# Optimization experiments

Hardware: AMD Instinct MI355X
Metric: run time of the kernel (lower is better)

The kernel has to match this reference:

```python
import jax, jax.numpy as jnp
import numpy as np

E = 8
D_IN = 1024
D_HID = 4096
D_OUT = 1024
N_TOK = 32768  # total tokens; equal split of 4096 per expert


def setup_inputs() -> dict:
    key = jax.random.key(0)
    k_in, k_w1, k_w2 = jax.random.split(key, 3)
    inputs = jax.random.normal(k_in, (N_TOK, D_IN), dtype=jnp.float32)
    expert_size = jnp.full((E,), N_TOK // E, dtype=jnp.int64)
    # reset_parameters: normal(0, 1/sqrt(fan_in)) per expert
    w1 = jax.random.normal(k_w1, (E, D_IN, D_HID), dtype=jnp.float32) / np.sqrt(D_IN)
    b1 = jnp.zeros((E, D_HID), dtype=jnp.float32)
    w2 = jax.random.normal(k_w2, (E, D_HID, D_OUT), dtype=jnp.float32) / np.sqrt(D_HID)
    b2 = jnp.zeros((E, D_OUT), dtype=jnp.float32)
    return {"inputs": inputs, "expert_size": expert_size,
            "w1": w1, "b1": b1, "w2": w2, "b2": b2}


def reference(inputs, expert_size, w1, b1, w2, b2):
    # Grouped GEMM over contiguous per-expert splits. expert_size is equal
    # per expert (N_TOK // E), so the variable-split loop in the torch code
    # collapses to a batched einsum with identical math.
    e = w1.shape[0]
    n, d = inputs.shape
    cap = n // e  # tokens per expert (equal splits)
    x = inputs.reshape(e, cap, d)                       # [E, cap, D_IN]
    h = jnp.einsum('ecd,edh->ech', x, w1) + b1[:, None, :]
    h = jax.nn.gelu(h, approximate=False)               # F.gelu default = erf gelu
    y = jnp.einsum('ech,eho->eco', h, w2) + b2[:, None, :]
    return y.reshape(n, -1)                             # [N_TOK, D_OUT]
```

## Files before the change

kernel.cpp:

```cpp
#include <hip/hip_runtime.h>
#include <hip/hip_bf16.h>
#include <type_traits>

#define NE 8
#define DIN 1024
#define DHID 4096
#define DOUTD 1024
#define NTOK 32768
#define CAP (NTOK / NE)

typedef unsigned short u16;
typedef __attribute__((ext_vector_type(8))) short bf16x8;
typedef __attribute__((ext_vector_type(4))) float f32x4;

template <int I> using ic = std::integral_constant<int, I>;

__device__ __forceinline__ u16 f2bf(float x) {
  unsigned u = __builtin_bit_cast(unsigned, x);
  u += 0x7fffu + ((u >> 16) & 1u);
  return (u16)(u >> 16);
}

__device__ __forceinline__ float gelu_f(float x) {
  float u = 0.7978845608028654f * x * (1.0f + 0.044715f * x * x);
  float t = __expf(-2.0f * fabsf(u));
  float r = __fdividef(2.0f * t, 1.0f + t);
  float th = copysignf(1.0f - r, u);
  return 0.5f * x * (1.0f + th);
}

__device__ __forceinline__ void async_ld16(const void* g, void* l) {
  __builtin_amdgcn_global_load_lds(
      (const __attribute__((address_space(1))) unsigned int*)g,
      (__attribute__((address_space(3))) unsigned int*)l, 16, 0, 0);
}

__global__ __launch_bounds__(256) void convert_bf16_kernel(const float* __restrict__ in,
                                                           u16* __restrict__ out) {
  size_t i = ((size_t)blockIdx.x * 256 + threadIdx.x) * 8;
  float4 a = *(const float4*)(in + i);
  float4 b = *(const float4*)(in + i + 4);
  uint4 o;
  o.x = (unsigned)f2bf(a.x) | ((unsigned)f2bf(a.y) << 16);
  o.y = (unsigned)f2bf(a.z) | ((unsigned)f2bf(a.w) << 16);
  o.z = (unsigned)f2bf(b.x) | ((unsigned)f2bf(b.y) << 16);
  o.w = (unsigned)f2bf(b.z) | ((unsigned)f2bf(b.w) << 16);
  *(uint4*)(out + i) = o;
}

__global__ __launch_bounds__(256) void transpose_bf16_kernel(const float* __restrict__ in,
                                                             u16* __restrict__ out,
                                                             int K, int N) {
  __shared__ __align__(16) u16 tile[64 * 72];
  const int e = blockIdx.z;
  const int n0 = blockIdx.x * 64;
  const int k0 = blockIdx.y * 64;
  const float* inp = in + (size_t)e * K * N;
  u16* outp = out + (size_t)e * N * K;
  const int t = threadIdx.x;
  const int kr = t >> 4;
  const int nc = (t & 15) * 4;
#pragma unroll
  for (int rr = 0; rr < 4; ++rr) {
    int kl = rr * 16 + kr;
    float4 v = *(const float4*)(inp + (size_t)(k0 + kl) * N + n0 + nc);
    tile[(nc + 0) * 72 + kl] = f2bf(v.x);
    tile[(nc + 1) * 72 + kl] = f2bf(v.y);
    tile[(nc + 2) * 72 + kl] = f2bf(v.z);
    tile[(nc + 3) * 72 + kl] = f2bf(v.w);
  }
  __syncthreads();
  const int nr = t >> 3;
  const int kc = (t & 7) * 8;
#pragma unroll
  for (int it = 0; it < 2; ++it) {
    int nl = it * 32 + nr;
    bf16x8 w = *(const bf16x8*)(tile + nl * 72 + kc);
    *(bf16x8*)(outp + (size_t)(n0 + nl) * K + k0 + kc) = w;
  }
}

template <int K, int N, bool GELU_OUT>
__global__ __launch_bounds__(256, 2) void moe_gemm128_kernel(
    const u16* __restrict__ A, const u16* __restrict__ Bt,
    const float* __restrict__ bias, void* __restrict__ Out) {
  extern __shared__ __align__(16) char smem_raw[];
  constexpr int TX = N / 128;
  constexpr int NT = K / 64;
  static_assert(NT % 2 == 0 && NT >= 4, "K-tile count");
  static_assert(TX % 8 == 0, "supertile map needs TX%8==0");

  const int bid = blockIdx.x;
  const int e = bid & 7;
  const int idx = bid >> 3;
  constexpr int STC = TX / 8;
  const int st = idx >> 6;
  const int win = idx & 63;
  const int m0 = ((st / STC) * 8 + (win >> 3)) * 128;
  const int n0 = ((st % STC) * 8 + (win & 7)) * 128;

  const u16* Ae = A + (size_t)e * CAP * K;
  const u16* Be = Bt + (size_t)e * N * K;

  const int tid = threadIdx.x;
  const int l = tid & 63;
  const int w = tid >> 6;
  const int wr = w >> 1;
  const int wc = w & 1;
  const int g = l >> 4;
  const int rl = l & 15;

  int aoff0[4], aoff1[4], boff0[4], boff1[4];
#pragma unroll
  for (int j = 0; j < 4; ++j) {
    int r = wr * 64 + j * 16 + rl;
    aoff0[j] = r * 128 + (((0 * 4 + g) ^ (r & 7)) << 4);
    aoff1[j] = r * 128 + (((1 * 4 + g) ^ (r & 7)) << 4);
  }
#pragma unroll
  for (int i = 0; i < 4; ++i) {
    int r = wc * 64 + i * 16 + rl;
    boff0[i] = 16384 + r * 128 + (((0 * 4 + g) ^ (r & 7)) << 4);
    boff1[i] = 16384 + r * 128 + (((1 * 4 + g) ^ (r & 7)) << 4);
  }

  auto mkoff = [&](int s, int base0) -> size_t {
    int lrow = s >> 3, pu = s & 7;
    int lu = pu ^ (lrow & 7);
    return (size_t)(base0 + lrow) * K + lu * 8;
  };
  const u16* pA[4];
  const u16* pB[4];
#pragma unroll
  for (int r = 0; r < 4; ++r) {
    pA[r] = Ae + mkoff(r * 256 + tid, m0);
    pB[r] = Be + mkoff(r * 256 + tid, n0);
  }
  const int dsl = tid * 16;

  f32x4 acc[4][4] = {};

#pragma unroll
  for (int r = 0; r < 4; ++r) async_ld16(pA[r], smem_raw + r * 4096 + dsl);
#pragma unroll
  for (int r = 0; r < 4; ++r) async_ld16(pB[r], smem_raw + 16384 + r * 4096 + dsl);
  asm volatile("s_waitcnt vmcnt(0)\n\ts_barrier" ::: "memory");
  __builtin_amdgcn_sched_barrier(0);

  auto tile = [&](auto Jc, auto STc, auto LASTc) {
    constexpr int J = decltype(Jc)::value;
    constexpr bool STg = decltype(STc)::value;
    constexpr bool LAST = decltype(LASTc)::value;
    const char* bufr = smem_raw + J * 32768;
    char* bufs = (char*)smem_raw + (J ^ 1) * 32768;
    const int stE = (J + 1) * 64;
    if constexpr (STg) {
#pragma unroll
      for (int r = 0; r < 4; ++r) async_ld16(pA[r] + stE, bufs + r * 4096 + dsl);
#pragma unroll
      for (int r = 0; r < 4; ++r) async_ld16(pB[r] + stE, bufs + 16384 + r * 4096 + dsl);
    }
    bf16x8 b0[4], a0[4], b1[4], a1[4];
#pragma unroll
    for (int i = 0; i < 4; ++i) b0[i] = *(const bf16x8*)(bufr + boff0[i]);
#pragma unroll
    for (int j = 0; j < 4; ++j) a0[j] = *(const bf16x8*)(bufr + aoff0[j]);
#pragma unroll
    for (int i = 0; i < 4; ++i) b1[i] = *(const bf16x8*)(bufr + boff1[i]);
#pragma unroll
    for (int j = 0; j < 4; ++j) a1[j] = *(const bf16x8*)(bufr + aoff1[j]);
    asm volatile("s_waitcnt lgkmcnt(8)" ::: "memory");
    __builtin_amdgcn_sched_barrier(0);
    __builtin_amdgcn_s_setprio(1);
#pragma unroll
    for (int j = 0; j < 4; ++j)
#pragma unroll
      for (int i = 0; i < 4; ++i)
        acc[j][i] = __builtin_amdgcn_mfma_f32_16x16x32_bf16(b0[i], a0[j], acc[j][i], 0, 0, 0);
    asm volatile("s_waitcnt lgkmcnt(0)" ::: "memory");
    __builtin_amdgcn_sched_barrier(0);
#pragma unroll
    for (int j = 0; j < 4; ++j)
#pragma unroll
      for (int i = 0; i < 4; ++i)
        acc[j][i] = __builtin_amdgcn_mfma_f32_16x16x32_bf16(b1[i], a1[j], acc[j][i], 0, 0, 0);
    __builtin_amdgcn_s_setprio(0);
    if constexpr (!LAST) {
      asm volatile("s_waitcnt vmcnt(0)\n\ts_barrier" ::: "memory");
      __builtin_amdgcn_sched_barrier(0);
    }
  };

#pragma unroll 1
  for (int pr = 0; pr < NT / 2 - 1; ++pr) {
    tile(ic<0>{}, std::true_type{}, std::false_type{});
    tile(ic<1>{}, std::true_type{}, std::false_type{});
#pragma unroll
    for (int r = 0; r < 4; ++r) { pA[r] += 128; pB[r] += 128; }
  }
  tile(ic<0>{}, std::true_type{}, std::false_type{});
  tile(ic<1>{}, std::false_type{}, std::true_type{});

  const float* be = bias + (size_t)e * N;
  const int mb = m0 + wr * 64 + rl;
  const int nb = n0 + wc * 64 + g * 4;
  if constexpr (GELU_OUT) {
    u16* Oe = (u16*)Out + (size_t)e * (size_t)CAP * N;
#pragma unroll
    for (int j = 0; j < 4; ++j) {
      int m = mb + j * 16;
#pragma unroll
      for (int i = 0; i < 4; ++i) {
        int n = nb + i * 16;
        float4 bv = *(const float4*)(be + n);
        ushort4 o;
        o.x = f2bf(gelu_f(acc[j][i][0] + bv.x));
        o.y = f2bf(gelu_f(acc[j][i][1] + bv.y));
        o.z = f2bf(gelu_f(acc[j][i][2] + bv.z));
        o.w = f2bf(gelu_f(acc[j][i][3] + bv.w));
        *(ushort4*)(Oe + (size_t)m * N + n) = o;
      }
    }
  } else {
    float* Oe = (float*)Out + (size_t)e * (size_t)CAP * N;
#pragma unroll
    for (int j = 0; j < 4; ++j) {
      int m = mb + j * 16;
#pragma unroll
      for (int i = 0; i < 4; ++i) {
        int n = nb + i * 16;
        float4 bv = *(const float4*)(be + n);
        float4 o;
        o.x = acc[j][i][0] + bv.x;
        o.y = acc[j][i][1] + bv.y;
        o.z = acc[j][i][2] + bv.z;
        o.w = acc[j][i][3] + bv.w;
        *(float4*)(Oe + (size_t)m * N + n) = o;
      }
    }
  }
}

extern "C" void kernel_launch(void* const* d_in, const int* in_sizes, int n_in,
                              void* d_out, int out_size, void* d_ws, size_t ws_size,
                              hipStream_t stream) {
  const float* x  = (const float*)d_in[0];
  const float* w1 = (const float*)d_in[2];
  const float* b1 = (const float*)d_in[3];
  const float* w2 = (const float*)d_in[4];
  const float* b2 = (const float*)d_in[5];
  float* out = (float*)d_out;

  char* wsp = (char*)d_ws;
  u16* x_bf = (u16*)(wsp);
  u16* w1t  = (u16*)(wsp + (size_t)67108864);
  u16* w2t  = (u16*)(wsp + (size_t)134217728);
  u16* h    = (u16*)(wsp + (size_t)201326592);

  hipFuncSetAttribute(reinterpret_cast<const void*>(moe_gemm128_kernel<DIN, DHID, true>),
                      hipFuncAttributeMaxDynamicSharedMemorySize, 65536);
  hipFuncSetAttribute(reinterpret_cast<const void*>(moe_gemm128_kernel<DHID, DOUTD, false>),
                      hipFuncAttributeMaxDynamicSharedMemorySize, 65536);

  convert_bf16_kernel<<<(NTOK * DIN) / (256 * 8), 256, 0, stream>>>(x, x_bf);
  transpose_bf16_kernel<<<dim3(DHID / 64, DIN / 64, NE), 256, 0, stream>>>(w1, w1t, DIN, DHID);
  transpose_bf16_kernel<<<dim3(DOUTD / 64, DHID / 64, NE), 256, 0, stream>>>(w2, w2t, DHID, DOUTD);

  moe_gemm128_kernel<DIN, DHID, true>
      <<<dim3(NE * (CAP / 128) * (DHID / 128)), 256, 65536, stream>>>(x_bf, w1t, b1, h);
  moe_gemm128_kernel<DHID, DOUTD, false>
      <<<dim3(NE * (CAP / 128) * (DOUTD / 128)), 256, 65536, stream>>>(h, w2t, b2, out);
}
```

Measured before the change: 784.0 us.

## Enlarge GEMM block tile to 256x256 with 16 waves per block

Replaces the 128x128 tile, 4-wave GEMM with a 256x256 tile computed by 16 waves (1024 threads), and doubles LDS to 128 KB for the double-buffered tiles. The LDS layout and swizzle are reworked so each thread issues one async load per 32-column half of A and B, and fragment loads are split into two phases interleaved with the MFMAs. The goal is to raise arithmetic intensity and cut global/L2 traffic per FLOP. In exchange, occupancy drops to one block per CU because of the LDS size, and latency hiding now depends on intra-block barriers across 16 waves. The launch_bounds(1024,4) setting is also unreachable in practice.

```diff
diff --git a/kernel.cpp b/kernel.cpp
--- a/kernel.cpp
+++ b/kernel.cpp
@@ -81,23 +81,23 @@
 }
 
 template <int K, int N, bool GELU_OUT>
-__global__ __launch_bounds__(256, 2) void moe_gemm128_kernel(
+__global__ __launch_bounds__(1024, 4) void moe_gemm16w_kernel(
     const u16* __restrict__ A, const u16* __restrict__ Bt,
     const float* __restrict__ bias, void* __restrict__ Out) {
   extern __shared__ __align__(16) char smem_raw[];
-  constexpr int TX = N / 128;
+  constexpr int TX = N / 256;
   constexpr int NT = K / 64;
   static_assert(NT % 2 == 0 && NT >= 4, "K-tile count");
-  static_assert(TX % 8 == 0, "supertile map needs TX%8==0");
+  static_assert(TX == 4 || TX == 16, "supertile map assumes TX in {4,16}");
 
   const int bid = blockIdx.x;
   const int e = bid & 7;
   const int idx = bid >> 3;
-  constexpr int STC = TX / 8;
-  const int st = idx >> 6;
-  const int win = idx & 63;
-  const int m0 = ((st / STC) * 8 + (win >> 3)) * 128;
-  const int n0 = ((st % STC) * 8 + (win & 7)) * 128;
+  constexpr int STC = TX / 4;
+  const int st = idx >> 4;
+  const int win = idx & 15;
+  const int m0 = ((st / STC) * 4 + (win >> 2)) * 256;
+  const int n0 = ((st % STC) * 4 + (win & 3)) * 256;
 
   const u16* Ae = A + (size_t)e * CAP * K;
   const u16* Be = Bt + (size_t)e * N * K;
@@ -105,45 +105,43 @@
   const int tid = threadIdx.x;
   const int l = tid & 63;
   const int w = tid >> 6;
-  const int wr = w >> 1;
-  const int wc = w & 1;
+  const int wr = w >> 2;
+  const int wc = w & 3;
   const int g = l >> 4;
   const int rl = l & 15;
 
-  int aoff0[4], aoff1[4], boff0[4], boff1[4];
+  int aoff[4], boff[4];
 #pragma unroll
   for (int j = 0; j < 4; ++j) {
     int r = wr * 64 + j * 16 + rl;
-    aoff0[j] = r * 128 + (((0 * 4 + g) ^ (r & 7)) << 4);
-    aoff1[j] = r * 128 + (((1 * 4 + g) ^ (r & 7)) << 4);
+    int r7 = r & 127;
+    int lu = (r >> 7) * 4 + g;
+    aoff[j] = r7 * 128 + ((lu ^ (r7 & 7)) << 4);
   }
 #pragma unroll
   for (int i = 0; i < 4; ++i) {
     int r = wc * 64 + i * 16 + rl;
-    boff0[i] = 16384 + r * 128 + (((0 * 4 + g) ^ (r & 7)) << 4);
-    boff1[i] = 16384 + r * 128 + (((1 * 4 + g) ^ (r & 7)) << 4);
-  }
-
-  auto mkoff = [&](int s, int base0) -> size_t {
-    int lrow = s >> 3, pu = s & 7;
+    int r7 = r & 127;
+    int lu = (r >> 7) * 4 + g;
+    boff[i] = r7 * 128 + ((lu ^ (r7 & 7)) << 4);
+  }
+
+  auto mkoff = [&](int base0) -> size_t {
+    int lrow = tid >> 3, pu = tid & 7;
     int lu = pu ^ (lrow & 7);
-    return (size_t)(base0 + lrow) * K + lu * 8;
+    int r = lrow + ((lu & 4) << 5);
+    return (size_t)(base0 + r) * K + (lu & 3) * 8;
   };
-  const u16* pA[4];
-  const u16* pB[4];
-#pragma unroll
-  for (int r = 0; r < 4; ++r) {
-    pA[r] = Ae + mkoff(r * 256 + tid, m0);
-    pB[r] = Be + mkoff(r * 256 + tid, n0);
-  }
+  const u16* pA = Ae + mkoff(m0);
+  const u16* pB = Be + mkoff(n0);
   const int dsl = tid * 16;
 
   f32x4 acc[4][4] = {};
 
-#pragma unroll
-  for (int r = 0; r < 4; ++r) async_ld16(pA[r], smem_raw + r * 4096 + dsl);
-#pragma unroll
-  for (int r = 0; r < 4; ++r) async_ld16(pB[r], smem_raw + 16384 + r * 4096 + dsl);
+  async_ld16(pA, smem_raw + dsl);
+  async_ld16(pA + 32, smem_raw + 16384 + dsl);
+  async_ld16(pB, smem_raw + 32768 + dsl);
+  async_ld16(pB + 32, smem_raw + 49152 + dsl);
   asm volatile("s_waitcnt vmcnt(0)\n\ts_barrier" ::: "memory");
   __builtin_amdgcn_sched_barrier(0);
 
@@ -151,39 +149,39 @@
     constexpr int J = decltype(Jc)::value;
     constexpr bool STg = decltype(STc)::value;
     constexpr bool LAST = decltype(LASTc)::value;
-    const char* bufr = smem_raw + J * 32768;
-    char* bufs = (char*)smem_raw + (J ^ 1) * 32768;
+    const char* bufr = smem_raw + J * 65536;
+    char* bufs = (char*)smem_raw + (J ^ 1) * 65536;
     const int stE = (J + 1) * 64;
     if constexpr (STg) {
-#pragma unroll
-      for (int r = 0; r < 4; ++r) async_ld16(pA[r] + stE, bufs + r * 4096 + dsl);
-#pragma unroll
-      for (int r = 0; r < 4; ++r) async_ld16(pB[r] + stE, bufs + 16384 + r * 4096 + dsl);
-    }
-    bf16x8 b0[4], a0[4], b1[4], a1[4];
-#pragma unroll
-    for (int i = 0; i < 4; ++i) b0[i] = *(const bf16x8*)(bufr + boff0[i]);
-#pragma unroll
-    for (int j = 0; j < 4; ++j) a0[j] = *(const bf16x8*)(bufr + aoff0[j]);
-#pragma unroll
-    for (int i = 0; i < 4; ++i) b1[i] = *(const bf16x8*)(bufr + boff1[i]);
-#pragma unroll
-    for (int j = 0; j < 4; ++j) a1[j] = *(const bf16x8*)(bufr + aoff1[j]);
-    asm volatile("s_waitcnt lgkmcnt(8)" ::: "memory");
+      async_ld16(pA + stE, bufs + dsl);
+      async_ld16(pA + stE + 32, bufs + 16384 + dsl);
+      async_ld16(pB + stE, bufs + 32768 + dsl);
+      async_ld16(pB + stE + 32, bufs + 49152 + dsl);
+    }
+    bf16x8 bfr[4], afr[4];
+#pragma unroll
+    for (int i = 0; i < 4; ++i) bfr[i] = *(const bf16x8*)(bufr + 32768 + boff[i]);
+#pragma unroll
+    for (int j = 0; j < 4; ++j) afr[j] = *(const bf16x8*)(bufr + aoff[j]);
+    asm volatile("s_waitcnt lgkmcnt(0)" ::: "memory");
     __builtin_amdgcn_sched_barrier(0);
     __builtin_amdgcn_s_setprio(1);
 #pragma unroll
     for (int j = 0; j < 4; ++j)
 #pragma unroll
       for (int i = 0; i < 4; ++i)
-        acc[j][i] = __builtin_amdgcn_mfma_f32_16x16x32_bf16(b0[i], a0[j], acc[j][i], 0, 0, 0);
+        acc[j][i] = __builtin_amdgcn_mfma_f32_16x16x32_bf16(bfr[i], afr[j], acc[j][i], 0, 0, 0);
+#pragma unroll
+    for (int i = 0; i < 4; ++i) bfr[i] = *(const bf16x8*)(bufr + 49152 + boff[i]);
+#pragma unroll
+    for (int j = 0; j < 4; ++j) afr[j] = *(const bf16x8*)(bufr + 16384 + aoff[j]);
     asm volatile("s_waitcnt lgkmcnt(0)" ::: "memory");
     __builtin_amdgcn_sched_barrier(0);
 #pragma unroll
     for (int j = 0; j < 4; ++j)
 #pragma unroll
       for (int i = 0; i < 4; ++i)
-        acc[j][i] = __builtin_amdgcn_mfma_f32_16x16x32_bf16(b1[i], a1[j], acc[j][i], 0, 0, 0);
+        acc[j][i] = __builtin_amdgcn_mfma_f32_16x16x32_bf16(bfr[i], afr[j], acc[j][i], 0, 0, 0);
     __builtin_amdgcn_s_setprio(0);
     if constexpr (!LAST) {
       asm volatile("s_waitcnt vmcnt(0)\n\ts_barrier" ::: "memory");
@@ -195,8 +193,7 @@
   for (int pr = 0; pr < NT / 2 - 1; ++pr) {
     tile(ic<0>{}, std::true_type{}, std::false_type{});
     tile(ic<1>{}, std::true_type{}, std::false_type{});
-#pragma unroll
-    for (int r = 0; r < 4; ++r) { pA[r] += 128; pB[r] += 128; }
+    pA += 128; pB += 128;
   }
   tile(ic<0>{}, std::true_type{}, std::false_type{});
   tile(ic<1>{}, std::false_type{}, std::true_type{});
@@ -257,17 +254,17 @@
   u16* w2t  = (u16*)(wsp + (size_t)134217728);
   u16* h    = (u16*)(wsp + (size_t)201326592);
 
-  hipFuncSetAttribute(reinterpret_cast<const void*>(moe_gemm128_kernel<DIN, DHID, true>),
-                      hipFuncAttributeMaxDynamicSharedMemorySize, 65536);
-  hipFuncSetAttribute(reinterpret_cast<const void*>(moe_gemm128_kernel<DHID, DOUTD, false>),
-                      hipFuncAttributeMaxDynamicSharedMemorySize, 65536);
+  hipFuncSetAttribute(reinterpret_cast<const void*>(moe_gemm16w_kernel<DIN, DHID, true>),
+                      hipFuncAttributeMaxDynamicSharedMemorySize, 131072);
+  hipFuncSetAttribute(reinterpret_cast<const void*>(moe_gemm16w_kernel<DHID, DOUTD, false>),
+                      hipFuncAttributeMaxDynamicSharedMemorySize, 131072);
 
   convert_bf16_kernel<<<(NTOK * DIN) / (256 * 8), 256, 0, stream>>>(x, x_bf);
   transpose_bf16_kernel<<<dim3(DHID / 64, DIN / 64, NE), 256, 0, stream>>>(w1, w1t, DIN, DHID);
   transpose_bf16_kernel<<<dim3(DOUTD / 64, DHID / 64, NE), 256, 0, stream>>>(w2, w2t, DHID, DOUTD);
 
-  moe_gemm128_kernel<DIN, DHID, true>
-      <<<dim3(NE * (CAP / 128) * (DHID / 128)), 256, 65536, stream>>>(x_bf, w1t, b1, h);
-  moe_gemm128_kernel<DHID, DOUTD, false>
-      <<<dim3(NE * (CAP / 128) * (DOUTD / 128)), 256, 65536, stream>>>(h, w2t, b2, out);
-}
+  moe_gemm16w_kernel<DIN, DHID, true>
+      <<<dim3(NE * (CAP / 256) * (DHID / 256)), 1024, 131072, stream>>>(x_bf, w1t, b1, h);
+  moe_gemm16w_kernel<DHID, DOUTD, false>
+      <<<dim3(NE * (CAP / 256) * (DOUTD / 256)), 1024, 131072, stream>>>(h, w2t, b2, out);
+}
```

Result: no change. 772.1 us (-1.5%).
